# Kernel tuning notes

Hardware: AMD Instinct MI355X
Metric: run time of the kernel (lower is better)

The kernel has to match this reference:

```python
import jax, jax.numpy as jnp
import numpy as np

N_CLASS = 81          # 80 foreground classes + background (class 0)
R = 1000              # test-time RoIs from RPN
IMG_H, IMG_W = 600.0, 800.0   # original_size
SCORE_THRESH = 0.05
NMS_THRESH = 0.5
LOC_STD = jnp.array([0.1, 0.1, 0.2, 0.2], dtype=jnp.float32)
LOC_MEAN = jnp.zeros(4, dtype=jnp.float32)


def setup_inputs() -> dict:
    key = jax.random.key(0)
    k1, k2, k3, k4 = jax.random.split(key, 4)
    # rois in (ymin, xmin, ymax, xmax) within the image
    yx = jax.random.uniform(k1, (R, 2), dtype=jnp.float32) * jnp.array([IMG_H * 0.8, IMG_W * 0.8])
    hw = jax.random.uniform(k2, (R, 2), dtype=jnp.float32) * jnp.array([IMG_H * 0.2, IMG_W * 0.2]) + 1.0
    roi = jnp.concatenate([yx, yx + hw], axis=1)                       # [R, 4]
    roi_loc = jax.random.normal(k3, (R, N_CLASS * 4), dtype=jnp.float32)
    roi_score = jax.random.normal(k4, (R, N_CLASS), dtype=jnp.float32) * 2.0
    return {"roi": roi, "roi_loc": roi_loc, "roi_score": roi_score}


def _loc2bbox(roi, loc):
    # roi [R,4] (ymin,xmin,ymax,xmax); loc [R,C,4] (dy,dx,dh,dw) -> bbox [R,C,4]
    h = roi[:, 2] - roi[:, 0]
    w = roi[:, 3] - roi[:, 1]
    cy = roi[:, 0] + 0.5 * h
    cx = roi[:, 1] + 0.5 * w
    dy, dx, dh, dw = loc[..., 0], loc[..., 1], loc[..., 2], loc[..., 3]
    ctr_y = dy * h[:, None] + cy[:, None]
    ctr_x = dx * w[:, None] + cx[:, None]
    nh = jnp.exp(dh) * h[:, None]
    nw = jnp.exp(dw) * w[:, None]
    return jnp.stack([ctr_y - 0.5 * nh, ctr_x - 0.5 * nw,
                      ctr_y + 0.5 * nh, ctr_x + 0.5 * nw], axis=-1)


def _nms_per_class(boxes, scores):
    # boxes [R,4], scores [R] -> (sorted boxes, sorted scores, keep mask)
    order = jnp.argsort(-scores)
    b = boxes[order]
    s = scores[order]
    valid = s > SCORE_THRESH
    area = (b[:, 2] - b[:, 0]) * (b[:, 3] - b[:, 1])
    tl = jnp.maximum(b[:, None, :2], b[None, :, :2])
    br = jnp.minimum(b[:, None, 2:], b[None, :, 2:])
    wh = jnp.clip(br - tl, 0.0)
    inter = wh[..., 0] * wh[..., 1]
    iou = inter / (area[:, None] + area[None, :] - inter + 1e-9)   # [R,R]
    idx = jnp.arange(R)

    def body(i, keep):
        sup = keep[i] & (iou[i] > NMS_THRESH) & (idx > i)
        return keep & ~sup

    keep = jax.lax.fori_loop(0, R, body, valid)
    return b, s, keep


def reference(roi, roi_loc, roi_score):
    loc = roi_loc.reshape(R, N_CLASS, 4) * LOC_STD + LOC_MEAN
    bbox = _loc2bbox(roi, loc)                                   # [R, C, 4]
    # clamp: even coords (y) to [0, H], odd coords (x) to [0, W]
    hi = jnp.array([IMG_H, IMG_W, IMG_H, IMG_W], dtype=bbox.dtype)
    bbox = jnp.clip(bbox, 0.0, hi)
    prob = jax.nn.softmax(roi_score, axis=1)                     # [R, C]
    # per-class suppression, skipping background class 0
    boxes_c = jnp.swapaxes(bbox, 0, 1)[1:]                       # [C-1, R, 4]
    scores_c = prob.T[1:]                                        # [C-1, R]
    b, s, keep = jax.vmap(_nms_per_class)(boxes_c, scores_c)
    out = jnp.where(keep[..., None],
                    jnp.concatenate([b, s[..., None]], axis=-1), 0.0)  # [C-1, R, 5]
    labels = jnp.broadcast_to(jnp.arange(N_CLASS - 1, dtype=jnp.int32)[:, None], keep.shape)
    labels = jnp.where(keep, labels, -1)
    return out, labels
```

## Files before the change

kernel.cpp:

```cpp
#include <hip/hip_runtime.h>
#include <math.h>

#define R 1000
#define NC 81
#define MAXP 1024
#define NT 512
#define SUPMAX 512
#define WMAX 8

__global__ __launch_bounds__(256) void softmax_stats_kernel(
    const float* __restrict__ roi_score,
    float* __restrict__ wsmax,
    float* __restrict__ wsrcp)
{
    const int wid  = threadIdx.x >> 6;
    const int lane = threadIdx.x & 63;
    const int r    = blockIdx.x * 4 + wid;
    if (r >= R) return;
    const float* sc = roi_score + r * NC;
    float v0 = sc[lane];
    float v1 = (lane < NC - 64) ? sc[lane + 64] : -INFINITY;
    float m = fmaxf(v0, v1);
    #pragma unroll
    for (int off = 32; off > 0; off >>= 1)
        m = fmaxf(m, __shfl_xor(m, off, 64));
    float e = expf(v0 - m) + ((lane < NC - 64) ? expf(v1 - m) : 0.0f);
    #pragma unroll
    for (int off = 32; off > 0; off >>= 1)
        e += __shfl_xor(e, off, 64);
    if (lane == 0) {
        wsmax[r] = m;
        wsrcp[r] = 1.0f / e;
    }
}

__global__ __launch_bounds__(NT) void frcnn_class_kernel(
    const float* __restrict__ roi,
    const float* __restrict__ roi_loc,
    const float* __restrict__ roi_score,
    const float* __restrict__ wsmax,
    const float* __restrict__ wsrcp,
    float* __restrict__ out)
{
    const int c   = blockIdx.x + 1;
    const int tid = threadIdx.x;

    __shared__ float s_score[MAXP];
    __shared__ int   s_idx[MAXP];
    __shared__ float s_ss[MAXP];
    __shared__ float s_y0[MAXP], s_x0[MAXP], s_y1[MAXP], s_x1[MAXP], s_area[MAXP];
    __shared__ int   s_keepi[MAXP];
    __shared__ unsigned long long s_sup[SUPMAX * WMAX];
    __shared__ unsigned long long s_kw[WMAX];
    __shared__ int   s_cnt;

    if (tid == 0) s_cnt = 0;
    __syncthreads();

    for (int r = tid; r < R; r += NT) {
        float p = expf(roi_score[r * NC + c] - wsmax[r]) * wsrcp[r];
        if (p > 0.05f) {
            int slot = atomicAdd(&s_cnt, 1);
            s_score[slot] = p;
            s_idx[slot]   = r;
        }
    }
    __syncthreads();
    const int V = s_cnt;

    for (int p = tid; p < V; p += NT) {
        float sp = s_score[p];
        int   ip = s_idx[p];
        int rank = 0;
        for (int q = 0; q < V; ++q) {
            float sq = s_score[q];
            int   iq = s_idx[q];
            rank += (sq > sp) || (sq == sp && iq < ip);
        }
        float ry0 = roi[ip*4+0], rx0 = roi[ip*4+1];
        float ry1 = roi[ip*4+2], rx1 = roi[ip*4+3];
        float h = ry1 - ry0, w = rx1 - rx0;
        float cy = ry0 + 0.5f*h, cx = rx0 + 0.5f*w;
        const float* lp = roi_loc + (size_t)ip*(NC*4) + c*4;
        float dy = lp[0]*0.1f, dx = lp[1]*0.1f;
        float dh = lp[2]*0.2f, dw = lp[3]*0.2f;
        float ny = dy*h + cy, nx = dx*w + cx;
        float nh = expf(dh)*h, nw = expf(dw)*w;
        float y0 = ny - 0.5f*nh, x0 = nx - 0.5f*nw;
        float y1 = ny + 0.5f*nh, x1 = nx + 0.5f*nw;
        y0 = fminf(fmaxf(y0, 0.f), 600.f);
        x0 = fminf(fmaxf(x0, 0.f), 800.f);
        y1 = fminf(fmaxf(y1, 0.f), 600.f);
        x1 = fminf(fmaxf(x1, 0.f), 800.f);
        s_ss[rank] = sp;
        s_y0[rank] = y0; s_x0[rank] = x0; s_y1[rank] = y1; s_x1[rank] = x1;
        s_area[rank] = (y1 - y0) * (x1 - x0);
        s_keepi[rank] = 1;
    }
    __syncthreads();

    if (V > 0 && V <= SUPMAX) {
        const int W = (V + 63) >> 6;
        for (int i = tid; i < V; i += NT) {
            float ay0 = s_y0[i], ax0 = s_x0[i];
            float ay1 = s_y1[i], ax1 = s_x1[i];
            float aa  = s_area[i];
            for (int w = 0; w < W; ++w) {
                int j0 = w * 64;
                int js = (i + 1 > j0) ? i + 1 : j0;
                int je = (j0 + 64 < V) ? j0 + 64 : V;
                unsigned long long bits = 0ull;
                for (int j = js; j < je; ++j) {
                    float ty = fmaxf(ay0, s_y0[j]);
                    float tx = fmaxf(ax0, s_x0[j]);
                    float by = fminf(ay1, s_y1[j]);
                    float bx = fminf(ax1, s_x1[j]);
                    float hh = fmaxf(by - ty, 0.f);
                    float ww = fmaxf(bx - tx, 0.f);
                    float inter = hh * ww;
                    float iou = inter / (aa + s_area[j] - inter + 1e-9f);
                    if (iou > 0.5f) bits |= (1ull << (j - j0));
                }
                s_sup[i * W + w] = bits;
            }
        }
        __syncthreads();
        if (tid == 0) {
            unsigned long long kw[WMAX];
            #pragma unroll
            for (int w = 0; w < WMAX; ++w) {
                int full = V - w * 64;
                kw[w] = (full >= 64) ? ~0ull : (full > 0 ? ((1ull << full) - 1ull) : 0ull);
            }
            #pragma unroll
            for (int w = 0; w < WMAX; ++w) {
                if (w * 64 < V) {
                    unsigned long long cur = kw[w];
                    int lim = V - w * 64; if (lim > 64) lim = 64;
                    for (int b = 0; b < lim; ++b) {
                        if ((cur >> b) & 1ull) {
                            const unsigned long long* row = &s_sup[(w * 64 + b) * W];
                            cur &= ~row[w];
                            #pragma unroll
                            for (int w2 = 0; w2 < WMAX; ++w2) {
                                if (w2 > w) { if (w2 < W) kw[w2] &= ~row[w2]; }
                            }
                        }
                    }
                    kw[w] = cur;
                }
            }
            #pragma unroll
            for (int w = 0; w < WMAX; ++w) s_kw[w] = kw[w];
        }
        __syncthreads();
    } else if (V > SUPMAX) {
        for (int i = 0; i < V; ++i) {
            if (s_keepi[i]) {
                float ay0 = s_y0[i], ax0 = s_x0[i];
                float ay1 = s_y1[i], ax1 = s_x1[i];
                float aa  = s_area[i];
                for (int jj = i + 1 + tid; jj < V; jj += NT) {
                    float ty = fmaxf(ay0, s_y0[jj]);
                    float tx = fmaxf(ax0, s_x0[jj]);
                    float by = fminf(ay1, s_y1[jj]);
                    float bx = fminf(ax1, s_x1[jj]);
                    float hh = fmaxf(by - ty, 0.f);
                    float ww = fmaxf(bx - tx, 0.f);
                    float inter = hh * ww;
                    float iou = inter / (aa + s_area[jj] - inter + 1e-9f);
                    if (iou > 0.5f) s_keepi[jj] = 0;
                }
            }
            __syncthreads();
        }
    }

    const bool matrix_path = (V <= SUPMAX);
    float* out0 = out + (size_t)(c - 1) * R * 5;
    float* out1 = out + (size_t)80 * R * 5 + (size_t)(c - 1) * R;
    for (int p = tid; p < R; p += NT) {
        bool kept = false;
        if (p < V)
            kept = matrix_path ? (((s_kw[p >> 6] >> (p & 63)) & 1ull) != 0ull)
                               : (s_keepi[p] != 0);
        float y0 = 0.f, x0 = 0.f, y1 = 0.f, x1 = 0.f, s = 0.f, lab = -1.0f;
        if (kept) {
            y0 = s_y0[p]; x0 = s_x0[p]; y1 = s_y1[p]; x1 = s_x1[p];
            s  = s_ss[p];
            lab = (float)(c - 1);
        }
        out0[p*5+0] = y0; out0[p*5+1] = x0; out0[p*5+2] = y1;
        out0[p*5+3] = x1; out0[p*5+4] = s;
        out1[p] = lab;
    }
}

extern "C" void kernel_launch(void* const* d_in, const int* in_sizes, int n_in,
                              void* d_out, int out_size, void* d_ws, size_t ws_size,
                              hipStream_t stream) {
    const float* roi       = (const float*)d_in[0];
    const float* roi_loc   = (const float*)d_in[1];
    const float* roi_score = (const float*)d_in[2];
    float* out   = (float*)d_out;
    float* wsmax = (float*)d_ws;
    float* wsrcp = wsmax + 1024;

    hipLaunchKernelGGL(softmax_stats_kernel, dim3((R + 3) / 4), dim3(256), 0, stream,
                       roi_score, wsmax, wsrcp);
    hipLaunchKernelGGL(frcnn_class_kernel, dim3(NC - 1), dim3(NT), 0, stream,
                       roi, roi_loc, roi_score, wsmax, wsrcp, out);
}
```

Baseline: 87.68 us.

## Compact above-threshold candidates per class in softmax kernel via global atomics

The softmax kernel now computes full probabilities and scatters each above-threshold (score, roi index) into per-class global buckets using atomic counters. The per-class NMS kernel reads only its compacted candidates instead of rescanning all 1000 RoIs with strided loads and exp. Block size drops from 512 to 256 threads. This adds a memset launch and global atomics, and the smaller block does less parallel work in the rank and IoU phases.

```diff
diff --git a/kernel.cpp b/kernel.cpp
--- a/kernel.cpp
+++ b/kernel.cpp
@@ -3,15 +3,16 @@
 
 #define R 1000
 #define NC 81
-#define MAXP 1024
-#define NT 512
+#define CAP 1024
+#define NTB 256
 #define SUPMAX 512
 #define WMAX 8
 
-__global__ __launch_bounds__(256) void softmax_stats_kernel(
+__global__ __launch_bounds__(256) void softmax_scatter_kernel(
     const float* __restrict__ roi_score,
-    float* __restrict__ wsmax,
-    float* __restrict__ wsrcp)
+    unsigned*    __restrict__ cnt,
+    float*       __restrict__ bs,
+    int*         __restrict__ bi)
 {
     const int wid  = threadIdx.x >> 6;
     const int lane = threadIdx.x & 63;
@@ -28,47 +29,52 @@
     #pragma unroll
     for (int off = 32; off > 0; off >>= 1)
         e += __shfl_xor(e, off, 64);
-    if (lane == 0) {
-        wsmax[r] = m;
-        wsrcp[r] = 1.0f / e;
+    float rcp = 1.0f / e;
+
+    float p0 = expf(v0 - m) * rcp;
+    if (lane >= 1 && p0 > 0.05f) {
+        unsigned pos = atomicAdd(&cnt[lane], 1u);
+        if (pos < CAP) { bs[lane * CAP + pos] = p0; bi[lane * CAP + pos] = r; }
+    }
+    if (lane < NC - 64) {
+        float p1 = expf(v1 - m) * rcp;
+        int c = lane + 64;
+        if (p1 > 0.05f) {
+            unsigned pos = atomicAdd(&cnt[c], 1u);
+            if (pos < CAP) { bs[c * CAP + pos] = p1; bi[c * CAP + pos] = r; }
+        }
     }
 }
 
-__global__ __launch_bounds__(NT) void frcnn_class_kernel(
+__global__ __launch_bounds__(NTB) void frcnn_class_kernel(
     const float* __restrict__ roi,
     const float* __restrict__ roi_loc,
-    const float* __restrict__ roi_score,
-    const float* __restrict__ wsmax,
-    const float* __restrict__ wsrcp,
+    const unsigned* __restrict__ cnt,
+    const float* __restrict__ bs,
+    const int*   __restrict__ bi,
     float* __restrict__ out)
 {
     const int c   = blockIdx.x + 1;
     const int tid = threadIdx.x;
 
-    __shared__ float s_score[MAXP];
-    __shared__ int   s_idx[MAXP];
-    __shared__ float s_ss[MAXP];
-    __shared__ float s_y0[MAXP], s_x0[MAXP], s_y1[MAXP], s_x1[MAXP], s_area[MAXP];
-    __shared__ int   s_keepi[MAXP];
+    __shared__ float s_score[CAP];
+    __shared__ int   s_idx[CAP];
+    __shared__ float s_ss[CAP];
+    __shared__ float s_y0[CAP], s_x0[CAP], s_y1[CAP], s_x1[CAP], s_area[CAP];
+    __shared__ int   s_keepi[CAP];
     __shared__ unsigned long long s_sup[SUPMAX * WMAX];
     __shared__ unsigned long long s_kw[WMAX];
-    __shared__ int   s_cnt;
-
-    if (tid == 0) s_cnt = 0;
+
+    unsigned vc = cnt[c];
+    const int V = (vc > CAP) ? CAP : (int)vc;
+
+    for (int t = tid; t < V; t += NTB) {
+        s_score[t] = bs[c * CAP + t];
+        s_idx[t]   = bi[c * CAP + t];
+    }
     __syncthreads();
 
-    for (int r = tid; r < R; r += NT) {
-        float p = expf(roi_score[r * NC + c] - wsmax[r]) * wsrcp[r];
-        if (p > 0.05f) {
-            int slot = atomicAdd(&s_cnt, 1);
-            s_score[slot] = p;
-            s_idx[slot]   = r;
-        }
-    }
-    __syncthreads();
-    const int V = s_cnt;
-
-    for (int p = tid; p < V; p += NT) {
+    for (int p = tid; p < V; p += NTB) {
         float sp = s_score[p];
         int   ip = s_idx[p];
         int rank = 0;
@@ -101,7 +107,7 @@
 
     if (V > 0 && V <= SUPMAX) {
         const int W = (V + 63) >> 6;
-        for (int i = tid; i < V; i += NT) {
+        for (int i = tid; i < V; i += NTB) {
             float ay0 = s_y0[i], ax0 = s_x0[i];
             float ay1 = s_y1[i], ax1 = s_x1[i];
             float aa  = s_area[i];
@@ -160,7 +166,7 @@
                 float ay0 = s_y0[i], ax0 = s_x0[i];
                 float ay1 = s_y1[i], ax1 = s_x1[i];
                 float aa  = s_area[i];
-                for (int jj = i + 1 + tid; jj < V; jj += NT) {
+                for (int jj = i + 1 + tid; jj < V; jj += NTB) {
                     float ty = fmaxf(ay0, s_y0[jj]);
                     float tx = fmaxf(ax0, s_x0[jj]);
                     float by = fminf(ay1, s_y1[jj]);
@@ -179,7 +185,7 @@
     const bool matrix_path = (V <= SUPMAX);
     float* out0 = out + (size_t)(c - 1) * R * 5;
     float* out1 = out + (size_t)80 * R * 5 + (size_t)(c - 1) * R;
-    for (int p = tid; p < R; p += NT) {
+    for (int p = tid; p < R; p += NTB) {
         bool kept = false;
         if (p < V)
             kept = matrix_path ? (((s_kw[p >> 6] >> (p & 63)) & 1ull) != 0ull)
@@ -202,12 +208,15 @@
     const float* roi       = (const float*)d_in[0];
     const float* roi_loc   = (const float*)d_in[1];
     const float* roi_score = (const float*)d_in[2];
-    float* out   = (float*)d_out;
-    float* wsmax = (float*)d_ws;
-    float* wsrcp = wsmax + 1024;
-
-    hipLaunchKernelGGL(softmax_stats_kernel, dim3((R + 3) / 4), dim3(256), 0, stream,
-                       roi_score, wsmax, wsrcp);
-    hipLaunchKernelGGL(frcnn_class_kernel, dim3(NC - 1), dim3(NT), 0, stream,
-                       roi, roi_loc, roi_score, wsmax, wsrcp, out);
+    float* out = (float*)d_out;
+
+    unsigned* cnt = (unsigned*)d_ws;
+    float*    bs  = (float*)((char*)d_ws + 512);
+    int*      bi  = (int*)((char*)d_ws + 512 + sizeof(float) * NC * CAP);
+
+    hipMemsetAsync(cnt, 0, NC * sizeof(unsigned), stream);
+    hipLaunchKernelGGL(softmax_scatter_kernel, dim3((R + 3) / 4), dim3(256), 0, stream,
+                       roi_score, cnt, bs, bi);
+    hipLaunchKernelGGL(frcnn_class_kernel, dim3(NC - 1), dim3(NTB), 0, stream,
+                       roi, roi_loc, cnt, bs, bi, out);
 }
```

Measured after the change: 99.77 us. 13.8% more time.
